# Optimization experiments

Hardware: AMD Instinct MI355X
Metric: run time of the kernel (lower is better)

Reference implementation:

```python
import jax, jax.numpy as jnp
import numpy as np

B, D, N = 1024, 2048, 30000
IOU_CLIP_LO, IOU_CLIP_HI = 0.2, 0.9


def _l2norm(x, axis=-1, eps=1e-12):
    return x / jnp.maximum(jnp.linalg.norm(x, axis=axis, keepdims=True), eps)


def setup_inputs() -> dict:
    key = jax.random.key(0)
    k1, k2, k3, k4, k5 = jax.random.split(key, 5)
    inputs = _l2norm(jax.random.normal(k1, (B, D), jnp.float32))
    features = _l2norm(jax.random.normal(k2, (N, D), jnp.float32))
    IoU = jax.random.uniform(k3, (B,), jnp.float32)
    indexes = jax.random.randint(k4, (B,), 0, N, dtype=jnp.int64)
    update_flag = jax.random.randint(k5, (B,), 0, 2, dtype=jnp.int32)
    return {"inputs": inputs, "features": features, "IoU": IoU,
            "indexes": indexes, "update_flag": update_flag}


def reference(inputs, features, IoU, indexes, update_flag):
    # Forward of HM.apply: similarity logits vs memory bank.
    outputs = inputs @ features.T  # [B, N]

    # Memory-bank update (side effect performed in HM.backward), update_method='max_iou':
    # sequential per-row conditional overwrite + L2 renorm; duplicates in `indexes`
    # must be processed in order, hence lax.scan.
    iou_c = jnp.clip(IoU, IOU_CLIP_LO, IOU_CLIP_HI)  # clamped as in backward (unused by max_iou)

    def step(feats, xs):
        x, y, iou, uf = xs
        row = feats[y]
        row = jnp.where(uf > 0, x, row)          # max_iou: overwrite if update_flag
        row = row / jnp.maximum(jnp.linalg.norm(row), 1e-12)  # row renorm (always)
        return feats.at[y].set(row), None

    new_features, _ = jax.lax.scan(step, features, (inputs, indexes, iou_c, update_flag))
    return outputs, new_features
```

## Files before the change

kernel.cpp:

```cpp
#include <hip/hip_runtime.h>
#include <stdint.h>

#define B_ROWS 1024
#define DDIM   2048
#define NFEAT  30000

#define BM 128
#define BN 128
#define BK 64

typedef __attribute__((ext_vector_type(8))) short short8;
typedef __attribute__((ext_vector_type(4))) float v4f;

typedef const __attribute__((address_space(1))) unsigned int* gptr_t;
typedef __attribute__((address_space(3))) unsigned int* lptr_t;

__device__ __forceinline__ unsigned short f32_to_bf16(float f) {
    unsigned int u = __float_as_uint(f);
    unsigned int r = u + 0x7FFFu + ((u >> 16) & 1u);
    return (unsigned short)(r >> 16);
}

__device__ __forceinline__ void async_copy16(const unsigned short* g, unsigned short* l) {
    __builtin_amdgcn_global_load_lds((gptr_t)g, (lptr_t)l, 16, 0, 0);
}

__global__ void f32_to_bf16_kernel(const float4* __restrict__ src,
                                   ushort4* __restrict__ dst, int n4) {
    int stride = gridDim.x * blockDim.x;
    for (int i = blockIdx.x * blockDim.x + threadIdx.x; i < n4; i += stride) {
        float4 v = src[i];
        ushort4 o;
        o.x = f32_to_bf16(v.x);
        o.y = f32_to_bf16(v.y);
        o.z = f32_to_bf16(v.z);
        o.w = f32_to_bf16(v.w);
        dst[i] = o;
    }
}

__global__ void copy_f32_kernel(const float4* __restrict__ src,
                                float4* __restrict__ dst, int n4) {
    int stride = gridDim.x * blockDim.x;
    for (int i = blockIdx.x * blockDim.x + threadIdx.x; i < n4; i += stride) {
        dst[i] = src[i];
    }
}

__global__ __launch_bounds__(256) void gemm_bf16_kernel(
    const unsigned short* __restrict__ A,
    const unsigned short* __restrict__ Bf,
    float* __restrict__ C)
{
    __shared__ unsigned short As[BM * BK];
    __shared__ unsigned short Bs[BN * BK];

    const int bid  = blockIdx.x;
    const int mblk = bid & 7;
    const int nblk = bid >> 3;
    const int tid  = threadIdx.x;
    const int wave = tid >> 6;
    const int lane = tid & 63;
    const int wm = wave & 1;
    const int wn = wave >> 1;

    const int ldrow = lane >> 3;
    const int ldcol = (lane & 7) * 8;

    const unsigned short* a_src[4];
    const unsigned short* b_src[4];
    unsigned short* a_dst[4];
    unsigned short* b_dst[4];
#pragma unroll
    for (int i = 0; i < 4; ++i) {
        int chunk = wave * 4 + i;
        int ar = mblk * BM + chunk * 8 + ldrow;
        int br = nblk * BN + chunk * 8 + ldrow;
        if (br >= NFEAT) br = NFEAT - 1;
        a_src[i] = A  + (size_t)ar * DDIM + ldcol;
        b_src[i] = Bf + (size_t)br * DDIM + ldcol;
        a_dst[i] = &As[chunk * 512];
        b_dst[i] = &Bs[chunk * 512];
    }

    v4f acc[4][4];
#pragma unroll
    for (int im = 0; im < 4; ++im)
#pragma unroll
        for (int in = 0; in < 4; ++in)
            acc[im][in] = (v4f){0.f, 0.f, 0.f, 0.f};

    for (int kt = 0; kt < DDIM / BK; ++kt) {
        __syncthreads();
#pragma unroll
        for (int i = 0; i < 4; ++i) {
            async_copy16(a_src[i] + kt * BK, a_dst[i]);
            async_copy16(b_src[i] + kt * BK, b_dst[i]);
        }
        __syncthreads();

#pragma unroll
        for (int kk = 0; kk < BK; kk += 32) {
            const int koff = kk + (lane >> 4) * 8;
            short8 afrag[4], bfrag[4];
#pragma unroll
            for (int im = 0; im < 4; ++im)
                afrag[im] = *(const short8*)&As[(wm * 64 + im * 16 + (lane & 15)) * BK + koff];
#pragma unroll
            for (int in = 0; in < 4; ++in)
                bfrag[in] = *(const short8*)&Bs[(wn * 64 + in * 16 + (lane & 15)) * BK + koff];
#pragma unroll
            for (int im = 0; im < 4; ++im)
#pragma unroll
                for (int in = 0; in < 4; ++in)
                    acc[im][in] = __builtin_amdgcn_mfma_f32_16x16x32_bf16(
                        afrag[im], bfrag[in], acc[im][in], 0, 0, 0);
        }
    }

    const int m_base = mblk * BM + wm * 64;
    const int n_base = nblk * BN + wn * 64;
#pragma unroll
    for (int im = 0; im < 4; ++im) {
        int m0 = m_base + im * 16 + (lane >> 4) * 4;
#pragma unroll
        for (int in = 0; in < 4; ++in) {
            int n = n_base + in * 16 + (lane & 15);
            if (n < NFEAT) {
#pragma unroll
                for (int r = 0; r < 4; ++r)
                    C[(size_t)(m0 + r) * NFEAT + n] = acc[im][in][r];
            }
        }
    }
}

__global__ void scatter_rows_kernel(const float* __restrict__ inputs,
                                    const int* __restrict__ idx,
                                    const int* __restrict__ uf,
                                    float* __restrict__ out_feats) {
    int b = blockIdx.x;
    if (uf[b] <= 0) return;
    int y = idx[b];
    __shared__ int dead;
    if (threadIdx.x == 0) dead = 0;
    __syncthreads();
    for (int b2 = b + 1 + threadIdx.x; b2 < B_ROWS; b2 += blockDim.x) {
        if (uf[b2] > 0 && idx[b2] == y) { dead = 1; break; }
    }
    __syncthreads();
    if (dead) return;
    const float4* s = (const float4*)(inputs + (size_t)b * DDIM);
    float4* d = (float4*)(out_feats + (size_t)y * DDIM);
    for (int i = threadIdx.x; i < DDIM / 4; i += blockDim.x) d[i] = s[i];
}

extern "C" void kernel_launch(void* const* d_in, const int* in_sizes, int n_in,
                              void* d_out, int out_size, void* d_ws, size_t ws_size,
                              hipStream_t stream) {
    const float* inputs   = (const float*)d_in[0];
    const float* features = (const float*)d_in[1];
    const int* indexes    = (const int*)d_in[3];
    const int* uf         = (const int*)d_in[4];

    float* out0 = (float*)d_out;
    float* out1 = out0 + (size_t)B_ROWS * NFEAT;

    unsigned short* featB = (unsigned short*)out1;
    unsigned short* inpB  = featB + (size_t)NFEAT * DDIM;

    const int nf4 = NFEAT * DDIM / 4;
    const int na4 = B_ROWS * DDIM / 4;

    f32_to_bf16_kernel<<<8192, 256, 0, stream>>>((const float4*)features, (ushort4*)featB, nf4);
    f32_to_bf16_kernel<<<2048, 256, 0, stream>>>((const float4*)inputs, (ushort4*)inpB, na4);

    const int n_nblk = (NFEAT + BN - 1) / BN;
    gemm_bf16_kernel<<<8 * n_nblk, 256, 0, stream>>>(inpB, featB, out0);

    copy_f32_kernel<<<8192, 256, 0, stream>>>((const float4*)features, (float4*)out1, nf4);
    scatter_rows_kernel<<<B_ROWS, 256, 0, stream>>>(inputs, indexes, uf, out1);
}
```

Baseline: 805.7 us.

## Replace GEMM with 256x256 8-phase pipelined kernel and fuse feature copy

Replaces the 128x128 single-buffered bf16 MFMA GEMM with a 256x256-tile, 512-thread kernel. The new kernel double-buffers 128KB of swizzled LDS, issues async global-to-LDS loads interleaved across eight MFMA phases, raises wave priority around the MFMAs, and remaps blocks across XCDs. When a workspace is available, the bf16 conversion of features is fused with the fp32 copy into the output, so features is read once instead of twice. The deeper pipeline and larger tile aim to hide memory latency and cut redundant operand loads, at the cost of heavy LDS and register use and fragile hand-placed waitcnt and barrier logic.

Result: faster. 670.9 us (-16.7%).

```diff
diff --git a/kernel.cpp b/kernel.cpp
--- a/kernel.cpp
+++ b/kernel.cpp
@@ -5,9 +5,13 @@
 #define DDIM   2048
 #define NFEAT  30000
 
-#define BM 128
-#define BN 128
+#define BM 256
+#define BN 256
 #define BK 64
+#define GRID_M 4
+#define GRID_N 118
+#define NBLOCKS (GRID_M * GRID_N)
+#define NKT (DDIM / BK)
 
 typedef __attribute__((ext_vector_type(8))) short short8;
 typedef __attribute__((ext_vector_type(4))) float v4f;
@@ -21,7 +25,7 @@
     return (unsigned short)(r >> 16);
 }
 
-__device__ __forceinline__ void async_copy16(const unsigned short* g, unsigned short* l) {
+__device__ __forceinline__ void async_copy16(const void* g, void* l) {
     __builtin_amdgcn_global_load_lds((gptr_t)g, (lptr_t)l, 16, 0, 0);
 }
 
@@ -39,6 +43,22 @@
     }
 }
 
+__global__ void fused_feat_kernel(const float4* __restrict__ src,
+                                  ushort4* __restrict__ dstB,
+                                  float4* __restrict__ dstF, int n4) {
+    int stride = gridDim.x * blockDim.x;
+    for (int i = blockIdx.x * blockDim.x + threadIdx.x; i < n4; i += stride) {
+        float4 v = src[i];
+        dstF[i] = v;
+        ushort4 o;
+        o.x = f32_to_bf16(v.x);
+        o.y = f32_to_bf16(v.y);
+        o.z = f32_to_bf16(v.z);
+        o.w = f32_to_bf16(v.w);
+        dstB[i] = o;
+    }
+}
+
 __global__ void copy_f32_kernel(const float4* __restrict__ src,
                                 float4* __restrict__ dst, int n4) {
     int stride = gridDim.x * blockDim.x;
@@ -47,92 +67,174 @@
     }
 }
 
-__global__ __launch_bounds__(256) void gemm_bf16_kernel(
+__global__ __launch_bounds__(512, 2) void gemm_bf16_8ph(
     const unsigned short* __restrict__ A,
     const unsigned short* __restrict__ Bf,
     float* __restrict__ C)
 {
-    __shared__ unsigned short As[BM * BK];
-    __shared__ unsigned short Bs[BN * BK];
-
-    const int bid  = blockIdx.x;
-    const int mblk = bid & 7;
-    const int nblk = bid >> 3;
+    __shared__ alignas(16) unsigned char lds[131072];
+
     const int tid  = threadIdx.x;
     const int wave = tid >> 6;
     const int lane = tid & 63;
-    const int wm = wave & 1;
-    const int wn = wave >> 1;
-
-    const int ldrow = lane >> 3;
-    const int ldcol = (lane & 7) * 8;
-
-    const unsigned short* a_src[4];
-    const unsigned short* b_src[4];
-    unsigned short* a_dst[4];
-    unsigned short* b_dst[4];
-#pragma unroll
-    for (int i = 0; i < 4; ++i) {
-        int chunk = wave * 4 + i;
-        int ar = mblk * BM + chunk * 8 + ldrow;
-        int br = nblk * BN + chunk * 8 + ldrow;
-        if (br >= NFEAT) br = NFEAT - 1;
-        a_src[i] = A  + (size_t)ar * DDIM + ldcol;
-        b_src[i] = Bf + (size_t)br * DDIM + ldcol;
-        a_dst[i] = &As[chunk * 512];
-        b_dst[i] = &Bs[chunk * 512];
-    }
-
-    v4f acc[4][4];
-#pragma unroll
-    for (int im = 0; im < 4; ++im)
-#pragma unroll
-        for (int in = 0; in < 4; ++in)
-            acc[im][in] = (v4f){0.f, 0.f, 0.f, 0.f};
-
-    for (int kt = 0; kt < DDIM / BK; ++kt) {
-        __syncthreads();
-#pragma unroll
-        for (int i = 0; i < 4; ++i) {
-            async_copy16(a_src[i] + kt * BK, a_dst[i]);
-            async_copy16(b_src[i] + kt * BK, b_dst[i]);
-        }
-        __syncthreads();
-
-#pragma unroll
-        for (int kk = 0; kk < BK; kk += 32) {
-            const int koff = kk + (lane >> 4) * 8;
-            short8 afrag[4], bfrag[4];
-#pragma unroll
-            for (int im = 0; im < 4; ++im)
-                afrag[im] = *(const short8*)&As[(wm * 64 + im * 16 + (lane & 15)) * BK + koff];
-#pragma unroll
-            for (int in = 0; in < 4; ++in)
-                bfrag[in] = *(const short8*)&Bs[(wn * 64 + in * 16 + (lane & 15)) * BK + koff];
-#pragma unroll
-            for (int im = 0; im < 4; ++im)
-#pragma unroll
-                for (int in = 0; in < 4; ++in)
-                    acc[im][in] = __builtin_amdgcn_mfma_f32_16x16x32_bf16(
-                        afrag[im], bfrag[in], acc[im][in], 0, 0, 0);
-        }
-    }
-
-    const int m_base = mblk * BM + wm * 64;
-    const int n_base = nblk * BN + wn * 64;
-#pragma unroll
-    for (int im = 0; im < 4; ++im) {
-        int m0 = m_base + im * 16 + (lane >> 4) * 4;
-#pragma unroll
-        for (int in = 0; in < 4; ++in) {
-            int n = n_base + in * 16 + (lane & 15);
-            if (n < NFEAT) {
+    const int wm   = wave >> 2;
+    const int wn   = wave & 3;
+    const int bh   = wn >> 1;
+
+    const int bid  = blockIdx.x;
+    const int wgid = (bid & 7) * (NBLOCKS / 8) + (bid >> 3);
+    const int mblk = wgid & (GRID_M - 1);
+    const int nblk = wgid >> 2;
+
+    const unsigned char* Ab = (const unsigned char*)A;
+    const unsigned char* Bb = (const unsigned char*)Bf;
+
+    size_t a_src[2][2], b_src[2][2];
+    int ld_off[2];
+#pragma unroll
+    for (int j = 0; j < 2; ++j) {
+        const int P = (wave + j * 8) * 1024 + lane * 16;
+        const int Q = P ^ (((P >> 9) & 1) << 5);
+        const int kh  = Q >> 13;
+        const int row = (Q >> 6) & 127;
+        const int cb  = Q & 63;
+        ld_off[j] = (wave + j * 8) * 1024;
+#pragma unroll
+        for (int h = 0; h < 2; ++h) {
+            const int ga = mblk * BM + h * 128 + row;
+            int gb = nblk * BN + h * 128 + row;
+            if (gb >= NFEAT) gb = NFEAT - 1;
+            a_src[h][j] = (size_t)ga * (DDIM * 2) + kh * 64 + cb;
+            b_src[h][j] = (size_t)gb * (DDIM * 2) + kh * 64 + cb;
+        }
+    }
+
+#define STAGE_A(kt, h) do {                                                         \
+    unsigned char* _d = &lds[((((kt) & 1) * 2 + (h)) << 14)];                       \
+    async_copy16(Ab + a_src[h][0] + (size_t)(kt) * 128, _d + ld_off[0]);            \
+    async_copy16(Ab + a_src[h][1] + (size_t)(kt) * 128, _d + ld_off[1]);            \
+} while (0)
+
+#define STAGE_B(kt, h) do {                                                         \
+    unsigned char* _d = &lds[65536 + ((((kt) & 1) * 2 + (h)) << 14)];               \
+    async_copy16(Bb + b_src[h][0] + (size_t)(kt) * 128, _d + ld_off[0]);            \
+    async_copy16(Bb + b_src[h][1] + (size_t)(kt) * 128, _d + ld_off[1]);            \
+} while (0)
+
+    int aoff[4], boff[4];
+#pragma unroll
+    for (int j = 0; j < 4; ++j) {
+        const int ar = j * 32 + wm * 16 + (lane & 15);
+        const int aq = ar * 64 + (lane >> 4) * 16;
+        aoff[j] = aq ^ (((ar >> 3) & 1) << 5);
+        const int br = (wn & 1) * 64 + j * 16 + (lane & 15);
+        const int bq = br * 64 + (lane >> 4) * 16;
+        boff[j] = bq ^ (((br >> 3) & 1) << 5);
+    }
+
+#define READ_A(slot, f, ks) \
+    (*(const short8*)&lds[((((slot) * 2) + ((f) >> 2)) << 14) + (ks) * 8192 + aoff[(f) & 3]])
+#define READ_B(slot, n, ks) \
+    (*(const short8*)&lds[65536 + ((((slot) * 2) + bh) << 14) + (ks) * 8192 + boff[n]])
+
+    v4f acc[8][4];
+#pragma unroll
+    for (int f = 0; f < 8; ++f)
+#pragma unroll
+        for (int n = 0; n < 4; ++n)
+            acc[f][n] = (v4f){0.f, 0.f, 0.f, 0.f};
+
+    short8 af[2][2];
+    short8 bfr[4][2];
+
+#define MFMA_QUAD(f0) do {                                                                             \
+    _Pragma("unroll")                                                                                  \
+    for (int n = 0; n < 4; ++n) {                                                                      \
+        acc[(f0)][n]     = __builtin_amdgcn_mfma_f32_16x16x32_bf16(af[0][0], bfr[n][0], acc[(f0)][n],     0, 0, 0); \
+        acc[(f0)][n]     = __builtin_amdgcn_mfma_f32_16x16x32_bf16(af[0][1], bfr[n][1], acc[(f0)][n],     0, 0, 0); \
+        acc[(f0) + 1][n] = __builtin_amdgcn_mfma_f32_16x16x32_bf16(af[1][0], bfr[n][0], acc[(f0) + 1][n], 0, 0, 0); \
+        acc[(f0) + 1][n] = __builtin_amdgcn_mfma_f32_16x16x32_bf16(af[1][1], bfr[n][1], acc[(f0) + 1][n], 0, 0, 0); \
+    }                                                                                                  \
+} while (0)
+
+    STAGE_B(0, 0); STAGE_B(0, 1); STAGE_A(0, 0); STAGE_A(0, 1);
+    STAGE_B(1, 0); STAGE_B(1, 1); STAGE_A(1, 0);
+    asm volatile("s_waitcnt vmcnt(6)" ::: "memory");
+    __builtin_amdgcn_s_barrier();
+
+    for (int t = 0; t < NKT; ++t) {
+        const int slot = t & 1;
+
+        af[0][0] = READ_A(slot, 0, 0); af[0][1] = READ_A(slot, 0, 1);
+        af[1][0] = READ_A(slot, 1, 0); af[1][1] = READ_A(slot, 1, 1);
+#pragma unroll
+        for (int n = 0; n < 4; ++n) {
+            bfr[n][0] = READ_B(slot, n, 0);
+            bfr[n][1] = READ_B(slot, n, 1);
+        }
+        if (t + 1 < NKT) STAGE_A(t + 1, 1);
+        asm volatile("s_waitcnt lgkmcnt(8)" ::: "memory");
+        __builtin_amdgcn_s_barrier();
+        asm volatile("s_waitcnt lgkmcnt(0)" ::: "memory");
+        __builtin_amdgcn_s_setprio(1);
+        MFMA_QUAD(0);
+        __builtin_amdgcn_s_setprio(0);
+        __builtin_amdgcn_s_barrier();
+
+        af[0][0] = READ_A(slot, 2, 0); af[0][1] = READ_A(slot, 2, 1);
+        af[1][0] = READ_A(slot, 3, 0); af[1][1] = READ_A(slot, 3, 1);
+        if (t + 2 < NKT) STAGE_B(t + 2, 0);
+        __builtin_amdgcn_s_barrier();
+        asm volatile("s_waitcnt lgkmcnt(0)" ::: "memory");
+        __builtin_amdgcn_s_setprio(1);
+        MFMA_QUAD(2);
+        __builtin_amdgcn_s_setprio(0);
+        __builtin_amdgcn_s_barrier();
+
+        af[0][0] = READ_A(slot, 4, 0); af[0][1] = READ_A(slot, 4, 1);
+        af[1][0] = READ_A(slot, 5, 0); af[1][1] = READ_A(slot, 5, 1);
+        if (t + 2 < NKT) STAGE_B(t + 2, 1);
+        __builtin_amdgcn_s_barrier();
+        asm volatile("s_waitcnt lgkmcnt(0)" ::: "memory");
+        __builtin_amdgcn_s_setprio(1);
+        MFMA_QUAD(4);
+        __builtin_amdgcn_s_setprio(0);
+        __builtin_amdgcn_s_barrier();
+
+        af[0][0] = READ_A(slot, 6, 0); af[0][1] = READ_A(slot, 6, 1);
+        af[1][0] = READ_A(slot, 7, 0); af[1][1] = READ_A(slot, 7, 1);
+        if (t + 2 < NKT) STAGE_A(t + 2, 0);
+        __builtin_amdgcn_s_barrier();
+        asm volatile("s_waitcnt lgkmcnt(0)" ::: "memory");
+        __builtin_amdgcn_s_setprio(1);
+        MFMA_QUAD(6);
+        __builtin_amdgcn_s_setprio(0);
+        if (t < NKT - 2) {
+            asm volatile("s_waitcnt vmcnt(6)" ::: "memory");
+        } else if (t == NKT - 2) {
+            asm volatile("s_waitcnt vmcnt(0)" ::: "memory");
+        }
+        __builtin_amdgcn_s_barrier();
+    }
+
+#pragma unroll
+    for (int f = 0; f < 8; ++f) {
+        const int gr = mblk * BM + f * 32 + wm * 16 + (lane >> 4) * 4;
+#pragma unroll
+        for (int n = 0; n < 4; ++n) {
+            const int gc = nblk * BN + wn * 64 + n * 16 + (lane & 15);
+            if (gc < NFEAT) {
 #pragma unroll
                 for (int r = 0; r < 4; ++r)
-                    C[(size_t)(m0 + r) * NFEAT + n] = acc[im][in][r];
+                    C[(size_t)(gr + r) * NFEAT + gc] = acc[f][n][r];
             }
         }
     }
+#undef STAGE_A
+#undef STAGE_B
+#undef READ_A
+#undef READ_B
+#undef MFMA_QUAD
 }
 
 __global__ void scatter_rows_kernel(const float* __restrict__ inputs,
@@ -166,18 +268,29 @@
     float* out0 = (float*)d_out;
     float* out1 = out0 + (size_t)B_ROWS * NFEAT;
 
-    unsigned short* featB = (unsigned short*)out1;
-    unsigned short* inpB  = featB + (size_t)NFEAT * DDIM;
-
     const int nf4 = NFEAT * DDIM / 4;
     const int na4 = B_ROWS * DDIM / 4;
 
-    f32_to_bf16_kernel<<<8192, 256, 0, stream>>>((const float4*)features, (ushort4*)featB, nf4);
-    f32_to_bf16_kernel<<<2048, 256, 0, stream>>>((const float4*)inputs, (ushort4*)inpB, na4);
-
-    const int n_nblk = (NFEAT + BN - 1) / BN;
-    gemm_bf16_kernel<<<8 * n_nblk, 256, 0, stream>>>(inpB, featB, out0);
-
-    copy_f32_kernel<<<8192, 256, 0, stream>>>((const float4*)features, (float4*)out1, nf4);
-    scatter_rows_kernel<<<B_ROWS, 256, 0, stream>>>(inputs, indexes, uf, out1);
-}
+    const size_t featB_bytes = (size_t)NFEAT * DDIM * 2;
+    const size_t inpB_bytes  = (size_t)B_ROWS * DDIM * 2;
+
+    if (d_ws && ws_size >= featB_bytes + inpB_bytes) {
+        unsigned short* featB = (unsigned short*)d_ws;
+        unsigned short* inpB  = (unsigned short*)((char*)d_ws + featB_bytes);
+
+        fused_feat_kernel<<<4096, 256, 0, stream>>>((const float4*)features,
+                                                    (ushort4*)featB, (float4*)out1, nf4);
+        f32_to_bf16_kernel<<<2048, 256, 0, stream>>>((const float4*)inputs, (ushort4*)inpB, na4);
+        gemm_bf16_8ph<<<NBLOCKS, 512, 0, stream>>>(inpB, featB, out0);
+        scatter_rows_kernel<<<B_ROWS, 256, 0, stream>>>(inputs, indexes, uf, out1);
+    } else {
+        unsigned short* featB = (unsigned short*)out1;
+        unsigned short* inpB  = featB + (size_t)NFEAT * DDIM;
+
+        f32_to_bf16_kernel<<<8192, 256, 0, stream>>>((const float4*)features, (ushort4*)featB, nf4);
+        f32_to_bf16_kernel<<<2048, 256, 0, stream>>>((const float4*)inputs, (ushort4*)inpB, na4);
+        gemm_bf16_8ph<<<NBLOCKS, 512, 0, stream>>>(inpB, featB, out0);
+        copy_f32_kernel<<<8192, 256, 0, stream>>>((const float4*)features, (float4*)out1, nf4);
+        scatter_rows_kernel<<<B_ROWS, 256, 0, stream>>>(inputs, indexes, uf, out1);
+    }
+}
```
